# Kernel optimization log

Measured on AMD Instinct MI355X. Metric: run time of the kernel, lower is better.

Reference implementation:

```python
import jax, jax.numpy as jnp
import numpy as np

NUM_HEADS = 8
N_POINTS = 9
OFFSET_SCALE = 4.0


def bilinear_sample(fmap_flat, xy, H, W):
    """fmap_flat: (BH, H*W, C) row-major spatial; xy: (BH, S, 2) pixel coords (x, y).
    grid_sample(mode='bilinear', padding_mode='zeros', align_corners=True) equivalent.
    Returns (BH, S, C)."""
    x, y = xy[..., 0], xy[..., 1]
    x0 = jnp.floor(x); y0 = jnp.floor(y)
    x1 = x0 + 1.0;    y1 = y0 + 1.0
    wx1 = x - x0; wx0 = 1.0 - wx1
    wy1 = y - y0; wy0 = 1.0 - wy1

    def corner(xi, yi, wgt):
        valid = (xi >= 0) & (xi <= W - 1) & (yi >= 0) & (yi <= H - 1)
        xi_c = jnp.clip(xi, 0, W - 1).astype(jnp.int32)
        yi_c = jnp.clip(yi, 0, H - 1).astype(jnp.int32)
        idx = yi_c * W + xi_c                                   # (BH, S)
        vals = jnp.take_along_axis(fmap_flat, idx[..., None], axis=1)  # (BH, S, C)
        return vals * (wgt * valid.astype(fmap_flat.dtype))[..., None]

    return (corner(x0, y0, wx0 * wy0) + corner(x1, y0, wx1 * wy0)
            + corner(x0, y1, wx0 * wy1) + corner(x1, y1, wx1 * wy1))


def setup_inputs() -> dict:
    key = jax.random.key(0)
    ks = jax.random.split(key, 10)
    B, N, D = 4, 6400, 256
    Hh, P = NUM_HEADS, N_POINTS
    s = 0.02
    return {
        "x":    jax.random.normal(ks[0], (B, N, D), dtype=jnp.float32),
        "Wq":   jax.random.normal(ks[1], (D, D), dtype=jnp.float32) * s,
        "bq":   jnp.zeros((D,), jnp.float32),
        "Woff": jax.random.normal(ks[2], (Hh * P * 2, D), dtype=jnp.float32) * s,
        "boff": jax.random.normal(ks[3], (Hh * P * 2,), dtype=jnp.float32) * s,
        "Wkv":  jax.random.normal(ks[4], (2 * D, D), dtype=jnp.float32) * s,
        "bkv":  jnp.zeros((2 * D,), jnp.float32),
        "Wout": jax.random.normal(ks[5], (D, D), dtype=jnp.float32) * s,
        "bout": jnp.zeros((D,), jnp.float32),
        "h": 40,
        "w": 160,
    }


def reference(x, Wq, bq, Woff, boff, Wkv, bkv, Wout, bout, h, w):
    B, N, D = x.shape
    H, P = NUM_HEADS, N_POINTS
    hd = D // H

    # queries: (B, H, N, hd)
    q = (x @ Wq.T + bq).reshape(B, N, H, hd).transpose(0, 2, 1, 3)

    # per-query per-head offsets in pixels: (B, N, H, P, 2) (dx, dy)
    offsets = jnp.tanh(x @ Woff.T + boff).reshape(B, N, H, P, 2) * OFFSET_SCALE

    # K/V feature maps via 1x1 conv == per-token linear; split heads, flat spatial
    kv = x @ Wkv.T + bkv                     # (B, N, 2D)
    k = kv[..., :D]
    v = kv[..., D:]
    k_flat = k.reshape(B, N, H, hd).transpose(0, 2, 1, 3).reshape(B * H, N, hd)
    v_flat = v.reshape(B, N, H, hd).transpose(0, 2, 1, 3).reshape(B * H, N, hd)

    # base pixel grid (x, y), row-major over (h, w)
    ys, xs = jnp.meshgrid(jnp.arange(h, dtype=x.dtype), jnp.arange(w, dtype=x.dtype), indexing="ij")
    base_xy = jnp.stack([xs, ys], axis=-1).reshape(N, 2)

    # sampling locations: (B, N, H, P, 2) -> (B*H, N*P, 2)
    sample_xy = base_xy[None, :, None, None, :] + offsets
    sample_xy = sample_xy.transpose(0, 2, 1, 3, 4).reshape(B * H, N * P, 2)

    sampled_k = bilinear_sample(k_flat, sample_xy, h, w).reshape(B, H, N, P, hd)
    sampled_v = bilinear_sample(v_flat, sample_xy, h, w).reshape(B, H, N, P, hd)

    logits = jnp.einsum("bhnd,bhnpd->bhnp", q, sampled_k) * (hd ** -0.5)
    attn = jax.nn.softmax(logits, axis=-1)
    out = jnp.einsum("bhnp,bhnpd->bhnd", attn, sampled_v)   # (B, H, N, hd)
    out = out.transpose(0, 2, 1, 3).reshape(B, N, D)
    return out @ Wout.T + bout
```

## Files before the change

kernel.cpp:

```cpp
#include <hip/hip_runtime.h>
#include <math.h>

#define BSZ    4
#define NTOK   6400
#define DMODEL 256
#define NHEAD  8
#define HDIM   32
#define NPTS   9
#define HSP    40
#define WSP    160
#define KDIM   256
#define MTOT   (BSZ*NTOK)

typedef short  short8  __attribute__((ext_vector_type(8)));
typedef float  floatx4 __attribute__((ext_vector_type(4)));
typedef float  f32x2   __attribute__((ext_vector_type(2)));

__device__ __forceinline__ ushort f2bf(float f) {
    uint u = __float_as_uint(f);
    u = (u + 0x7FFFu + ((u >> 16) & 1u)) >> 16;
    return (ushort)u;
}

__device__ __forceinline__ void unpack8v(uint4 u, f32x2* f) {
    f[0].x = __uint_as_float(u.x << 16); f[0].y = __uint_as_float(u.x & 0xFFFF0000u);
    f[1].x = __uint_as_float(u.y << 16); f[1].y = __uint_as_float(u.y & 0xFFFF0000u);
    f[2].x = __uint_as_float(u.z << 16); f[2].y = __uint_as_float(u.z & 0xFFFF0000u);
    f[3].x = __uint_as_float(u.w << 16); f[3].y = __uint_as_float(u.w & 0xFFFF0000u);
}

__device__ __forceinline__ float dot8(uint4 u, const f32x2* q2) {
    f32x2 a; a.x = 0.f; a.y = 0.f;
    f32x2 t;
    t.x = __uint_as_float(u.x << 16); t.y = __uint_as_float(u.x & 0xFFFF0000u);
    a += t * q2[0];
    t.x = __uint_as_float(u.y << 16); t.y = __uint_as_float(u.y & 0xFFFF0000u);
    a += t * q2[1];
    t.x = __uint_as_float(u.z << 16); t.y = __uint_as_float(u.z & 0xFFFF0000u);
    a += t * q2[2];
    t.x = __uint_as_float(u.w << 16); t.y = __uint_as_float(u.w & 0xFFFF0000u);
    a += t * q2[3];
    return a.x + a.y;
}

#define AS1C(p) ((const __attribute__((address_space(1))) void*)(p))
#define AS3(p)  ((__attribute__((address_space(3))) void*)(p))

__global__ __launch_bounds__(256) void cast_all(
    const float* __restrict__ x,   const float* __restrict__ Wq,
    const float* __restrict__ Woff,const float* __restrict__ Wkv,
    const float* __restrict__ Wout,
    ushort* __restrict__ xb, ushort* __restrict__ wf, ushort* __restrict__ woutb)
{
    const int bid = blockIdx.x;
    if (bid >= 6500 && bid < 6528) {
        const int i = (bid - 6500) * 1024 + threadIdx.x * 4;
        ushort4 z; z.x = 0; z.y = 0; z.z = 0; z.w = 0;
        *(ushort4*)(wf + 400 * 256 + i) = z;
        return;
    }
    const float* src; ushort* dst; int base;
    if      (bid < 6400) { src = x;    dst = xb;              base = bid; }
    else if (bid < 6464) { src = Wq;   dst = wf;              base = bid - 6400; }
    else if (bid < 6500) { src = Woff; dst = wf + 256 * 256;  base = bid - 6464; }
    else if (bid < 6656) { src = Wkv;  dst = wf + 512 * 256;  base = bid - 6528; }
    else                 { src = Wout; dst = woutb;           base = bid - 6656; }
    const int i = base * 1024 + threadIdx.x * 4;
    float4 v = *(const float4*)(src + i);
    ushort4 o;
    o.x = f2bf(v.x); o.y = f2bf(v.y); o.z = f2bf(v.z); o.w = f2bf(v.w);
    *(ushort4*)(dst + i) = o;
}

template <int MODE>
__global__ __launch_bounds__(256) void gemm_2ph(
    const ushort* __restrict__ Xb,
    const ushort* __restrict__ Wf,
    const float* __restrict__ bq, const float* __restrict__ boff,
    const float* __restrict__ bkv,
    ushort* __restrict__ qb, float* __restrict__ off,
    ushort* __restrict__ kfb, ushort* __restrict__ vfb,
    float* __restrict__ Yout)
{
    constexpr int NBN = (MODE == 0) ? 8 : 2;
    __shared__ ushort As[2][128 * 64];
    __shared__ ushort Bs[2][128 * 64];

    const int tid = threadIdx.x;
    const int bid = blockIdx.x;
    const int xcd = bid & 7;
    const int j   = bid >> 3;
    const int block_n = (j % NBN) * 128;
    const int block_m = (xcd * 25 + j / NBN) * 128;

    const int wave = tid >> 6, lane = tid & 63;
    const int wm = (wave >> 1) * 64, wn = (wave & 1) * 64;
    const int l15 = lane & 15, quad = lane >> 4;

    const int srow  = lane >> 3;
    const int sslot = (lane & 7) ^ srow;

    floatx4 acc[4][4];
    #pragma unroll
    for (int i = 0; i < 4; ++i)
        #pragma unroll
        for (int jj = 0; jj < 4; ++jj) {
            acc[i][jj][0] = 0.f; acc[i][jj][1] = 0.f;
            acc[i][jj][2] = 0.f; acc[i][jj][3] = 0.f;
        }

    auto stage = [&](int buf, int kt) {
        #pragma unroll
        for (int i = 0; i < 4; ++i) {
            const int rb = wave * 32 + i * 8;
            const ushort* sa = Xb + (size_t)(block_m + rb + srow) * KDIM + kt + sslot * 8;
            const ushort* sb = Wf + (size_t)(block_n + rb + srow) * KDIM + kt + sslot * 8;
            __builtin_amdgcn_global_load_lds(AS1C(sa), AS3(&As[buf][rb * 64]), 16, 0, 0);
            __builtin_amdgcn_global_load_lds(AS1C(sb), AS3(&Bs[buf][rb * 64]), 16, 0, 0);
        }
    };

    auto compute = [&](int buf) {
        #pragma unroll
        for (int ks2 = 0; ks2 < 2; ++ks2) {
            short8 af[4], bfr[4];
            #pragma unroll
            for (int f = 0; f < 4; ++f) {
                const int ra = wm + f * 16 + l15;
                const int rbb = wn + f * 16 + l15;
                const int sl = (((ks2 * 4 + quad) ^ (l15 & 7))) * 8;
                af[f]  = *(const short8*)&As[buf][ra * 64 + sl];
                bfr[f] = *(const short8*)&Bs[buf][rbb * 64 + sl];
            }
            #pragma unroll
            for (int fm = 0; fm < 4; ++fm)
                #pragma unroll
                for (int fn = 0; fn < 4; ++fn)
                    acc[fm][fn] = __builtin_amdgcn_mfma_f32_16x16x32_bf16(
                        af[fm], bfr[fn], acc[fm][fn], 0, 0, 0);
        }
    };

    stage(0, 0);
    __syncthreads();
    #pragma unroll
    for (int t = 0; t < 3; ++t) {
        stage((t + 1) & 1, (t + 1) * 64);
        compute(t & 1);
        __syncthreads();
    }
    compute(1);

    #pragma unroll
    for (int fn = 0; fn < 4; ++fn) {
        const int col = block_n + wn + fn * 16 + l15;
        float bcol;
        if (MODE == 1) {
            bcol = bq[col];
        } else {
            if      (col < 256) bcol = bq[col];
            else if (col < 400) bcol = boff[col - 256];
            else if (col < 512) bcol = 0.f;
            else                bcol = bkv[col - 512];
        }
        #pragma unroll
        for (int fm = 0; fm < 4; ++fm) {
            #pragma unroll
            for (int r = 0; r < 4; ++r) {
                const int row = block_m + wm + fm * 16 + quad * 4 + r;
                const float val = acc[fm][fn][r] + bcol;
                if (MODE == 1) {
                    Yout[(size_t)row * DMODEL + col] = val;
                } else {
                    if (col < 256) {
                        qb[(size_t)row * DMODEL + col] = f2bf(val);
                    } else if (col < 400) {
                        off[(size_t)row * 144 + (col - 256)] = tanhf(val) * 4.0f;
                    } else if (col >= 512) {
                        const int c2 = col - 512;
                        const int bb = row / NTOK, nn = row % NTOK;
                        const int hh = (c2 & 255) >> 5, cc = c2 & 31;
                        const size_t o = (((size_t)(bb * NHEAD + hh)) * NTOK + nn) * HDIM + cc;
                        if (c2 < 256) kfb[o] = f2bf(val);
                        else          vfb[o] = f2bf(val);
                    }
                }
            }
        }
    }
}

__global__ __launch_bounds__(256) void deform_attn(
    const ushort* __restrict__ qb,
    const float* __restrict__ off,
    const ushort* __restrict__ kfb,
    const ushort* __restrict__ vfb,
    ushort* __restrict__ attnb)
{
    const int lane = threadIdx.x & 63;
    const int token = blockIdx.x * 8 + (threadIdx.x >> 6) * 2 + (lane >> 5);
    const int h = (lane >> 2) & 7, lc = lane & 3;
    const int b = token / NTOK, n = token % NTOK;

    const uint4 qu = *(const uint4*)(qb + (size_t)token * DMODEL + h * HDIM + lc * 8);
    f32x2 q2[4]; unpack8v(qu, q2);

    const float* ob = off + (size_t)token * 144 + h * (NPTS * 2);
    const float bx = (float)(n % WSP), by = (float)(n / WSP);
    const ushort* kbase = kfb + (size_t)(b * NHEAD + h) * NTOK * HDIM + lc * 8;
    const ushort* vbase = vfb + (size_t)(b * NHEAD + h) * NTOK * HDIM + lc * 8;

    float m = -INFINITY, s = 0.f;
    f32x2 o2[4];
    #pragma unroll
    for (int i = 0; i < 4; ++i) { o2[i].x = 0.f; o2[i].y = 0.f; }

    #pragma unroll
    for (int g = 0; g < 3; ++g) {
        int   idx[3][4];
        float wt[3][4];
        #pragma unroll
        for (int jj = 0; jj < 3; ++jj) {
            const int p = g * 3 + jj;
            const float2 of = *(const float2*)(ob + 2 * p);
            const float sx = bx + of.x, sy = by + of.y;
            const float fx0 = floorf(sx), fy0 = floorf(sy);
            const float wx1 = sx - fx0, wx0 = 1.0f - wx1;
            const float wy1 = sy - fy0, wy0 = 1.0f - wy1;
            const int ix0 = (int)fx0, iy0 = (int)fy0;
            const int ix1 = ix0 + 1, iy1 = iy0 + 1;
            const bool vx0 = (ix0 >= 0) & (ix0 <= WSP - 1);
            const bool vx1 = (ix1 >= 0) & (ix1 <= WSP - 1);
            const bool vy0 = (iy0 >= 0) & (iy0 <= HSP - 1);
            const bool vy1 = (iy1 >= 0) & (iy1 <= HSP - 1);
            const int cx0 = min(max(ix0, 0), WSP - 1);
            const int cx1 = min(max(ix1, 0), WSP - 1);
            const int cy0 = min(max(iy0, 0), HSP - 1);
            const int cy1 = min(max(iy1, 0), HSP - 1);
            wt[jj][0] = wx0 * wy0 * (float)(vx0 && vy0);
            wt[jj][1] = wx1 * wy0 * (float)(vx1 && vy0);
            wt[jj][2] = wx0 * wy1 * (float)(vx0 && vy1);
            wt[jj][3] = wx1 * wy1 * (float)(vx1 && vy1);
            idx[jj][0] = (cy0 * WSP + cx0) * HDIM;
            idx[jj][1] = (cy0 * WSP + cx1) * HDIM;
            idx[jj][2] = (cy1 * WSP + cx0) * HDIM;
            idx[jj][3] = (cy1 * WSP + cx1) * HDIM;
        }

        float l[3];
        #pragma unroll
        for (int jj = 0; jj < 3; ++jj) {
            const uint4 k0 = *(const uint4*)(kbase + idx[jj][0]);
            const uint4 k1 = *(const uint4*)(kbase + idx[jj][1]);
            const uint4 k2 = *(const uint4*)(kbase + idx[jj][2]);
            const uint4 k3 = *(const uint4*)(kbase + idx[jj][3]);
            float part = wt[jj][0] * dot8(k0, q2) + wt[jj][1] * dot8(k1, q2)
                       + wt[jj][2] * dot8(k2, q2) + wt[jj][3] * dot8(k3, q2);
            part += __shfl_xor(part, 1, 64);
            part += __shfl_xor(part, 2, 64);
            l[jj] = part * 0.17677669529663687f;
        }

        const float m1 = fmaxf(fmaxf(fmaxf(l[0], l[1]), l[2]), m);
        const float corr = __expf(m - m1);
        const float e0 = __expf(l[0] - m1);
        const float e1 = __expf(l[1] - m1);
        const float e2 = __expf(l[2] - m1);
        s = s * corr + e0 + e1 + e2;
        m = m1;
        const float e[3] = {e0, e1, e2};

        #pragma unroll
        for (int i = 0; i < 4; ++i) o2[i] *= corr;

        #pragma unroll
        for (int jj = 0; jj < 3; ++jj) {
            #pragma unroll
            for (int c = 0; c < 4; ++c) {
                const uint4 vu = *(const uint4*)(vbase + idx[jj][c]);
                f32x2 vv[4]; unpack8v(vu, vv);
                const float ew = e[jj] * wt[jj][c];
                #pragma unroll
                for (int i = 0; i < 4; ++i) o2[i] += vv[i] * ew;
            }
        }
    }

    const float inv = 1.0f / s;
    uint4 ru;
    ru.x = (uint)f2bf(o2[0].x * inv) | ((uint)f2bf(o2[0].y * inv) << 16);
    ru.y = (uint)f2bf(o2[1].x * inv) | ((uint)f2bf(o2[1].y * inv) << 16);
    ru.z = (uint)f2bf(o2[2].x * inv) | ((uint)f2bf(o2[2].y * inv) << 16);
    ru.w = (uint)f2bf(o2[3].x * inv) | ((uint)f2bf(o2[3].y * inv) << 16);
    *(uint4*)(attnb + (size_t)token * DMODEL + h * HDIM + lc * 8) = ru;
}

extern "C" void kernel_launch(void* const* d_in, const int* in_sizes, int n_in,
                              void* d_out, int out_size, void* d_ws, size_t ws_size,
                              hipStream_t stream) {
    const float* x    = (const float*)d_in[0];
    const float* Wq   = (const float*)d_in[1];
    const float* bq   = (const float*)d_in[2];
    const float* Woff = (const float*)d_in[3];
    const float* boff = (const float*)d_in[4];
    const float* Wkv  = (const float*)d_in[5];
    const float* bkv  = (const float*)d_in[6];
    const float* Wout = (const float*)d_in[7];
    const float* bout = (const float*)d_in[8];

    ushort* xb    = (ushort*)d_ws;
    ushort* qb    = xb + (size_t)MTOT * DMODEL;
    float*  off   = (float*)(qb + (size_t)MTOT * DMODEL);
    ushort* kfb   = (ushort*)(off + (size_t)MTOT * 144);
    ushort* vfb   = kfb + (size_t)MTOT * DMODEL;
    ushort* wf    = vfb + (size_t)MTOT * DMODEL;
    ushort* woutb = wf + 262144;
    ushort* attnb = xb;

    cast_all<<<dim3(6720), dim3(256), 0, stream>>>(x, Wq, Woff, Wkv, Wout,
                                                   xb, wf, woutb);

    gemm_2ph<0><<<dim3(1600), dim3(256), 0, stream>>>(xb, wf, bq, boff, bkv,
                                                      qb, off, kfb, vfb, nullptr);

    deform_attn<<<dim3(3200), dim3(256), 0, stream>>>(qb, off, kfb, vfb, attnb);

    gemm_2ph<1><<<dim3(400), dim3(256), 0, stream>>>(attnb, woutb, bout,
                                                     nullptr, nullptr, nullptr,
                                                     nullptr, nullptr, nullptr,
                                                     (float*)d_out);
}
```

Measured before the change: 218.5 us.

## Triple-buffer GEMM LDS pipeline, coarsen cast kernel, hoist token index division

The GEMM moves from two LDS stages to three, with explicit vmcnt waits and raw barriers, so two global-to-LDS loads stay in flight while each tile is computed. The cast kernel now handles four float4 chunks per thread with a quarter of the blocks, which cuts launch and scheduling overhead. The per-element row/NTOK division in the K/V scatter is replaced by a batch index computed once per block. In exchange the GEMM uses more LDS (96KB), which may lower occupancy, and the correctness of the hand-written vmcnt(8) counts depends on how many loads each stage issues.

New measurement: 248.1 us. +13.6%, slower.

```diff
diff --git a/kernel.cpp b/kernel.cpp
--- a/kernel.cpp
+++ b/kernel.cpp
@@ -53,27 +53,35 @@
     ushort* __restrict__ xb, ushort* __restrict__ wf, ushort* __restrict__ woutb)
 {
     const int bid = blockIdx.x;
-    if (bid >= 6500 && bid < 6528) {
-        const int i = (bid - 6500) * 1024 + threadIdx.x * 4;
+    if (bid >= 1625 && bid < 1632) {
+        const int i = (bid - 1625) * 4096 + threadIdx.x * 4;
         ushort4 z; z.x = 0; z.y = 0; z.z = 0; z.w = 0;
-        *(ushort4*)(wf + 400 * 256 + i) = z;
+        #pragma unroll
+        for (int k = 0; k < 4; ++k)
+            *(ushort4*)(wf + 400 * 256 + i + k * 1024) = z;
         return;
     }
     const float* src; ushort* dst; int base;
-    if      (bid < 6400) { src = x;    dst = xb;              base = bid; }
-    else if (bid < 6464) { src = Wq;   dst = wf;              base = bid - 6400; }
-    else if (bid < 6500) { src = Woff; dst = wf + 256 * 256;  base = bid - 6464; }
-    else if (bid < 6656) { src = Wkv;  dst = wf + 512 * 256;  base = bid - 6528; }
-    else                 { src = Wout; dst = woutb;           base = bid - 6656; }
-    const int i = base * 1024 + threadIdx.x * 4;
-    float4 v = *(const float4*)(src + i);
-    ushort4 o;
-    o.x = f2bf(v.x); o.y = f2bf(v.y); o.z = f2bf(v.z); o.w = f2bf(v.w);
-    *(ushort4*)(dst + i) = o;
+    if      (bid < 1600) { src = x;    dst = xb;              base = bid; }
+    else if (bid < 1616) { src = Wq;   dst = wf;              base = bid - 1600; }
+    else if (bid < 1625) { src = Woff; dst = wf + 256 * 256;  base = bid - 1616; }
+    else if (bid < 1664) { src = Wkv;  dst = wf + 512 * 256;  base = bid - 1632; }
+    else                 { src = Wout; dst = woutb;           base = bid - 1664; }
+    const int i0 = base * 4096 + threadIdx.x * 4;
+    float4 v[4];
+    #pragma unroll
+    for (int k = 0; k < 4; ++k) v[k] = *(const float4*)(src + i0 + k * 1024);
+    #pragma unroll
+    for (int k = 0; k < 4; ++k) {
+        ushort4 o;
+        o.x = f2bf(v[k].x); o.y = f2bf(v[k].y);
+        o.z = f2bf(v[k].z); o.w = f2bf(v[k].w);
+        *(ushort4*)(dst + i0 + k * 1024) = o;
+    }
 }
 
 template <int MODE>
-__global__ __launch_bounds__(256) void gemm_2ph(
+__global__ __launch_bounds__(256) void gemm_3buf(
     const ushort* __restrict__ Xb,
     const ushort* __restrict__ Wf,
     const float* __restrict__ bq, const float* __restrict__ boff,
@@ -83,8 +91,8 @@
     float* __restrict__ Yout)
 {
     constexpr int NBN = (MODE == 0) ? 8 : 2;
-    __shared__ ushort As[2][128 * 64];
-    __shared__ ushort Bs[2][128 * 64];
+    __shared__ ushort As[3][128 * 64];
+    __shared__ ushort Bs[3][128 * 64];
 
     const int tid = threadIdx.x;
     const int bid = blockIdx.x;
@@ -142,15 +150,28 @@
     };
 
     stage(0, 0);
-    __syncthreads();
-    #pragma unroll
-    for (int t = 0; t < 3; ++t) {
-        stage((t + 1) & 1, (t + 1) * 64);
-        compute(t & 1);
-        __syncthreads();
-    }
+    stage(1, 64);
+    asm volatile("s_waitcnt vmcnt(8)" ::: "memory");
+    __builtin_amdgcn_s_barrier();
+
+    stage(2, 128);
+    compute(0);
+    asm volatile("s_waitcnt vmcnt(8)" ::: "memory");
+    __builtin_amdgcn_s_barrier();
+
+    stage(0, 192);
     compute(1);
-
+    asm volatile("s_waitcnt vmcnt(8)" ::: "memory");
+    __builtin_amdgcn_s_barrier();
+
+    compute(2);
+    asm volatile("s_waitcnt vmcnt(0)" ::: "memory");
+    __builtin_amdgcn_s_barrier();
+
+    compute(0);
+
+    const int bb  = block_m / NTOK;
+    const int nn0 = block_m - bb * NTOK;
     #pragma unroll
     for (int fn = 0; fn < 4; ++fn) {
         const int col = block_n + wn + fn * 16 + l15;
@@ -178,8 +199,8 @@
                         off[(size_t)row * 144 + (col - 256)] = tanhf(val) * 4.0f;
                     } else if (col >= 512) {
                         const int c2 = col - 512;
-                        const int bb = row / NTOK, nn = row % NTOK;
                         const int hh = (c2 & 255) >> 5, cc = c2 & 31;
+                        const int nn = nn0 + wm + fm * 16 + quad * 4 + r;
                         const size_t o = (((size_t)(bb * NHEAD + hh)) * NTOK + nn) * HDIM + cc;
                         if (c2 < 256) kfb[o] = f2bf(val);
                         else          vfb[o] = f2bf(val);
@@ -317,16 +338,16 @@
     ushort* woutb = wf + 262144;
     ushort* attnb = xb;
 
-    cast_all<<<dim3(6720), dim3(256), 0, stream>>>(x, Wq, Woff, Wkv, Wout,
+    cast_all<<<dim3(1680), dim3(256), 0, stream>>>(x, Wq, Woff, Wkv, Wout,
                                                    xb, wf, woutb);
 
-    gemm_2ph<0><<<dim3(1600), dim3(256), 0, stream>>>(xb, wf, bq, boff, bkv,
-                                                      qb, off, kfb, vfb, nullptr);
+    gemm_3buf<0><<<dim3(1600), dim3(256), 0, stream>>>(xb, wf, bq, boff, bkv,
+                                                       qb, off, kfb, vfb, nullptr);
 
     deform_attn<<<dim3(3200), dim3(256), 0, stream>>>(qb, off, kfb, vfb, attnb);
 
-    gemm_2ph<1><<<dim3(400), dim3(256), 0, stream>>>(attnb, woutb, bout,
-                                                     nullptr, nullptr, nullptr,
-                                                     nullptr, nullptr, nullptr,
-                                                     (float*)d_out);
-}
+    gemm_3buf<1><<<dim3(400), dim3(256), 0, stream>>>(attnb, woutb, bout,
+                                                      nullptr, nullptr, nullptr,
+                                                      nullptr, nullptr, nullptr,
+                                                      (float*)d_out);
+}
```
